# Kernel optimization log

Hardware: AMD Instinct MI355X
Metric: run time of the kernel (lower is better)

The kernel has to match this reference:

```python
import jax, jax.numpy as jnp
import numpy as np

N = 100000   # num nodes
E = 1600000  # num edges (before self loops)
D = 128      # feature / hidden dim
H = 256      # mlp hidden
L = 40       # num labels


def setup_inputs() -> dict:
    key = jax.random.key(0)
    ks = jax.random.split(key, 12)
    x = jax.random.normal(ks[0], (N, D), dtype=jnp.float32)
    edge_index = jax.random.randint(ks[1], (2, E), 0, N, dtype=jnp.int32)
    def glorot(k, shape):
        lim = float(np.sqrt(6.0 / (shape[0] + shape[1])))
        return jax.random.uniform(k, shape, jnp.float32, -lim, lim)
    params = {
        "W0": glorot(ks[2], (D, D)), "b0": jnp.zeros((D,), jnp.float32),
        "W1": glorot(ks[3], (D, D)), "b1": jnp.zeros((D,), jnp.float32),
        "W2": glorot(ks[4], (D, D)), "b2": jnp.zeros((D,), jnp.float32),
        "Wm1": glorot(ks[5], (D, H)), "bm1": jnp.zeros((H,), jnp.float32),
        "Wm2": glorot(ks[6], (H, L)), "bm2": jnp.zeros((L,), jnp.float32),
    }
    return {"x": x, "edge_index": edge_index, **params}


def _gcn_norm(edge_index):
    # add self loops (renorm trick), symmetric normalization D^-1/2 A D^-1/2
    self_loops = jnp.arange(N, dtype=edge_index.dtype)
    row = jnp.concatenate([edge_index[0], self_loops])
    col = jnp.concatenate([edge_index[1], self_loops])
    ones = jnp.ones(row.shape[0], jnp.float32)
    deg = jax.ops.segment_sum(ones, row, num_segments=N)
    dinv = jnp.where(deg > 0, jax.lax.rsqrt(deg), 0.0)
    norm_w = dinv[row] * dinv[col]  # [E+N]
    return row, col, norm_w


def _sage_layer(x, row, col, norm_w, W, b):
    msg = x[col] * norm_w[:, None]                      # [E+N, D] gather
    agg = jax.ops.segment_sum(msg, row, num_segments=N)  # [N, D] scatter-add
    return jax.nn.relu(agg @ W + b)


def reference(x, edge_index, W0, b0, W1, b1, W2, b2, Wm1, bm1, Wm2, bm2):
    row, col, norm_w = _gcn_norm(edge_index)
    h = _sage_layer(x, row, col, norm_w, W0, b0)
    h = _sage_layer(h, row, col, norm_w, W1, b1)
    h = _sage_layer(h, row, col, norm_w, W2, b2)
    h = jax.nn.relu(h @ Wm1 + bm1)  # Flatten is identity on [N, D]
    return h @ Wm2 + bm2            # [N, L] logits
```

## Files before the change

kernel.cpp:

```cpp
#include <hip/hip_runtime.h>
#include <hip/hip_bf16.h>
#include <stdint.h>

#define NN 100000
#define NE 1600000
#define DD 128
#define HH 256
#define LL 40

typedef __attribute__((ext_vector_type(8))) short short8;
typedef __attribute__((ext_vector_type(4))) float float4v;

__device__ __forceinline__ float bfu_lo(uint32_t u){ union{uint32_t i;float f;}v; v.i=u<<16; return v.f; }
__device__ __forceinline__ float bfu_hi(uint32_t u){ union{uint32_t i;float f;}v; v.i=u&0xFFFF0000u; return v.f; }
__device__ __forceinline__ float bf2f(uint16_t u){ union{uint32_t i;float f;}v; v.i=((uint32_t)u)<<16; return v.f; }
__device__ __forceinline__ uint16_t f2bf(float f){
  union{float f;uint32_t i;}v; v.f=f; uint32_t u=v.i;
  u += 0x7FFFu + ((u>>16)&1u); return (uint16_t)(u>>16);
}
__device__ __forceinline__ void split2(float f, short &hi, short &lo){
  uint16_t h = f2bf(f);
  hi = (short)h;
  lo = (short)f2bf(f - bf2f(h));
}
__device__ __forceinline__ float u2f(uint32_t u){ union{uint32_t i;float f;}v; v.i=u; return v.f; }


__global__ __launch_bounds__(256) void count_edges(const int* __restrict__ row,
                                                   int* __restrict__ counts, uint16_t* __restrict__ rank){
  int e = blockIdx.x*256 + threadIdx.x;
  if (e < NE) rank[e] = (uint16_t)atomicAdd(&counts[row[e]], 1);
}

__global__ __launch_bounds__(256) void scan_partial(const int* __restrict__ counts,
                                                    int* __restrict__ offs, int* __restrict__ bsums,
                                                    float* __restrict__ dinv){
  __shared__ int sh[256];
  int t = threadIdx.x, i = blockIdx.x*256 + t;
  int v = (i < NN) ? counts[i] : 0;
  if (i < NN) dinv[i] = rsqrtf((float)(v + 1));
  sh[t] = v; __syncthreads();
  for (int d = 1; d < 256; d <<= 1){
    int x = (t >= d) ? sh[t-d] : 0;
    __syncthreads();
    sh[t] += x;
    __syncthreads();
  }
  if (i < NN) offs[i] = sh[t] - v;
  if (t == 255) bsums[blockIdx.x] = sh[255];
}

__global__ __launch_bounds__(512) void scan_block(int* __restrict__ bsums, int nb){
  __shared__ int sh[512];
  int t = threadIdx.x;
  int v = (t < nb) ? bsums[t] : 0;
  sh[t] = v; __syncthreads();
  for (int d = 1; d < 512; d <<= 1){
    int x = (t >= d) ? sh[t-d] : 0;
    __syncthreads();
    sh[t] += x;
    __syncthreads();
  }
  if (t < nb) bsums[t] = sh[t] - v;
}

__global__ __launch_bounds__(256) void scan_add(int* __restrict__ offs, const int* __restrict__ bsums){
  int i = blockIdx.x*256 + threadIdx.x;
  if (i < NN) offs[i] += bsums[blockIdx.x];
  if (i == 0) offs[NN] = NE;
}

__global__ __launch_bounds__(256) void fill_csr(const int* __restrict__ row, const int* __restrict__ col,
                                                const uint16_t* __restrict__ rank,
                                                const int* __restrict__ offs,
                                                const float* __restrict__ dinv,
                                                uint2* __restrict__ csr_cw){
  int e = blockIdx.x*256 + threadIdx.x;
  if (e < NE){
    int r = row[e];
    int c = col[e];
    int p = offs[r] + (int)rank[e];
    uint2 v;
    v.x = (uint32_t)c;
    union{float f;uint32_t i;}w; w.f = dinv[c];
    v.y = w.i;
    csr_cw[p] = v;
  }
}

__global__ __launch_bounds__(256) void cvt_bf16(const float2* __restrict__ x, uint32_t* __restrict__ hb){
  int i = blockIdx.x*256 + threadIdx.x;
  if (i < NN*64){
    float2 v = x[i];
    hb[i] = (uint32_t)f2bf(v.x) | ((uint32_t)f2bf(v.y) << 16);
  }
}


template<int KDIM, int NCOL, int NTBP>
__global__ __launch_bounds__(256) void swz(const float* __restrict__ W, uint16_t* __restrict__ Wf){
  constexpr int KB = KDIM / 32;
  constexpr int TOT = KB * NTBP * 512;
  int idx = blockIdx.x*256 + threadIdx.x;
  if (idx >= TOT) return;
  int frag = idx >> 9, r = idx & 511, ln = r >> 3, j = r & 7;
  int kb = frag / NTBP, nt = frag - kb*NTBP;
  int k = kb*32 + ((ln >> 4) << 3) + j;
  int n = nt*16 + (ln & 15);
  float w = (n < NCOL) ? W[k*NCOL + n] : 0.f;
  Wf[idx] = f2bf(w);
}


__global__ __launch_bounds__(256) void agg_gemm(const uint32_t* __restrict__ hb,
                                                const int* __restrict__ offs,
                                                const uint2* __restrict__ csr_cw,
                                                const float* __restrict__ dinv,
                                                const uint16_t* __restrict__ Wf,
                                                const float* __restrict__ bias,
                                                uint16_t* __restrict__ Hout){
  __shared__ float lds[16*129];
  const int lane = threadIdx.x & 63;
  const int wid = threadIdx.x >> 6;
  const int rbase = blockIdx.x*16;

  for (int rl = wid*4; rl < wid*4 + 4; ++rl){
    const int w = rbase + rl;
    const int s = offs[w], e = offs[w+1];
    const float dr = dinv[w];
    const uint32_t us = hb[(size_t)w*64 + lane];

    float a0=0.f,a1=0.f,b0=0.f,b1=0.f,c0=0.f,c1=0.f,d0=0.f,d1=0.f;
    float e0=0.f,e1=0.f,f0=0.f,f1=0.f,g0=0.f,g1=0.f,h0=0.f,h1=0.f;
    int i = s;
    for (; i + 8 <= e; i += 8){
      uint2 p0=csr_cw[i],  p1=csr_cw[i+1], p2=csr_cw[i+2], p3=csr_cw[i+3];
      uint2 p4=csr_cw[i+4],p5=csr_cw[i+5], p6=csr_cw[i+6], p7=csr_cw[i+7];
      uint32_t u0=hb[(size_t)p0.x*64+lane], u1=hb[(size_t)p1.x*64+lane];
      uint32_t u2=hb[(size_t)p2.x*64+lane], u3=hb[(size_t)p3.x*64+lane];
      uint32_t u4=hb[(size_t)p4.x*64+lane], u5=hb[(size_t)p5.x*64+lane];
      uint32_t u6=hb[(size_t)p6.x*64+lane], u7=hb[(size_t)p7.x*64+lane];
      a0 += u2f(p0.y)*bfu_lo(u0); a1 += u2f(p0.y)*bfu_hi(u0);
      b0 += u2f(p1.y)*bfu_lo(u1); b1 += u2f(p1.y)*bfu_hi(u1);
      c0 += u2f(p2.y)*bfu_lo(u2); c1 += u2f(p2.y)*bfu_hi(u2);
      d0 += u2f(p3.y)*bfu_lo(u3); d1 += u2f(p3.y)*bfu_hi(u3);
      e0 += u2f(p4.y)*bfu_lo(u4); e1 += u2f(p4.y)*bfu_hi(u4);
      f0 += u2f(p5.y)*bfu_lo(u5); f1 += u2f(p5.y)*bfu_hi(u5);
      g0 += u2f(p6.y)*bfu_lo(u6); g1 += u2f(p6.y)*bfu_hi(u6);
      h0 += u2f(p7.y)*bfu_lo(u7); h1 += u2f(p7.y)*bfu_hi(u7);
    }
    if (i + 4 <= e){
      uint2 p0=csr_cw[i], p1=csr_cw[i+1], p2=csr_cw[i+2], p3=csr_cw[i+3];
      uint32_t u0=hb[(size_t)p0.x*64+lane], u1=hb[(size_t)p1.x*64+lane];
      uint32_t u2=hb[(size_t)p2.x*64+lane], u3=hb[(size_t)p3.x*64+lane];
      a0 += u2f(p0.y)*bfu_lo(u0); a1 += u2f(p0.y)*bfu_hi(u0);
      b0 += u2f(p1.y)*bfu_lo(u1); b1 += u2f(p1.y)*bfu_hi(u1);
      c0 += u2f(p2.y)*bfu_lo(u2); c1 += u2f(p2.y)*bfu_hi(u2);
      d0 += u2f(p3.y)*bfu_lo(u3); d1 += u2f(p3.y)*bfu_hi(u3);
      i += 4;
    }
    for (; i < e; ++i){
      uint2 p = csr_cw[i];
      uint32_t u = hb[(size_t)p.x*64 + lane];
      a0 += u2f(p.y)*bfu_lo(u); a1 += u2f(p.y)*bfu_hi(u);
    }
    float r0 = (((a0+b0)+(c0+d0)) + ((e0+f0)+(g0+h0))) + dr*bfu_lo(us);
    float r1 = (((a1+b1)+(c1+d1)) + ((e1+f1)+(g1+h1))) + dr*bfu_hi(us);
    lds[rl*129 + 2*lane]     = r0*dr;
    lds[rl*129 + 2*lane + 1] = r1*dr;
  }
  __syncthreads();

  const int mr = lane & 15;
  const int ko = (lane >> 4) << 3;
  float4v acc[2];
  { float4v z = {0.f,0.f,0.f,0.f}; acc[0] = z; acc[1] = z; }
#pragma unroll
  for (int kb = 0; kb < 4; ++kb){
    short8 ah, al;
#pragma unroll
    for (int j = 0; j < 8; ++j){
      float f = lds[mr*129 + kb*32 + ko + j];
      short h, l; split2(f, h, l); ah[j] = h; al[j] = l;
    }
#pragma unroll
    for (int t = 0; t < 2; ++t){
      int nt = wid*2 + t;
      short8 bf = *(const short8*)&Wf[(kb*8 + nt)*512 + lane*8];
      acc[t] = __builtin_amdgcn_mfma_f32_16x16x32_bf16(ah, bf, acc[t], 0, 0, 0);
      acc[t] = __builtin_amdgcn_mfma_f32_16x16x32_bf16(al, bf, acc[t], 0, 0, 0);
    }
  }
  const int col = lane & 15;
  const int rb  = (lane >> 4) * 4;
#pragma unroll
  for (int t = 0; t < 2; ++t){
    int n = (wid*2 + t)*16 + col;
    float bv = bias[n];
#pragma unroll
    for (int r = 0; r < 4; ++r){
      int m = rbase + rb + r;
      float v = acc[t][r] + bv;
      Hout[(size_t)m*128 + n] = f2bf(v > 0.f ? v : 0.f);
    }
  }
}


#define HS 260

__global__ __launch_bounds__(256) void mlp_fused(const uint16_t* __restrict__ Hb,
                                                 const uint16_t* __restrict__ W1f,
                                                 const float* __restrict__ b1,
                                                 const uint16_t* __restrict__ W2f,
                                                 const float* __restrict__ b2,
                                                 float* __restrict__ out, int M){
  __shared__ uint16_t hid[128*HS];
  const int lane = threadIdx.x & 63;
  const int wid = threadIdx.x >> 6;
  const int mbase = blockIdx.x*128 + wid*32;
  const int mr = lane & 15;
  const int a0r = (mbase + mr < M) ? (mbase + mr) : (M-1);
  const int a1r = (mbase + 16 + mr < M) ? (mbase + 16 + mr) : (M-1);
  const int ko = (lane >> 4) << 3;
  const int col = lane & 15;
  const int rb  = (lane >> 4) * 4;

  float4v acc1[16][2];
#pragma unroll
  for (int nt = 0; nt < 16; ++nt){ float4v z = {0.f,0.f,0.f,0.f}; acc1[nt][0] = z; acc1[nt][1] = z; }
#pragma unroll
  for (int kb = 0; kb < 4; ++kb){
    short8 af0 = *(const short8*)&Hb[(size_t)a0r*128 + kb*32 + ko];
    short8 af1 = *(const short8*)&Hb[(size_t)a1r*128 + kb*32 + ko];
#pragma unroll
    for (int nt = 0; nt < 16; ++nt){
      short8 bf = *(const short8*)&W1f[(kb*16 + nt)*512 + lane*8];
      acc1[nt][0] = __builtin_amdgcn_mfma_f32_16x16x32_bf16(af0, bf, acc1[nt][0], 0, 0, 0);
      acc1[nt][1] = __builtin_amdgcn_mfma_f32_16x16x32_bf16(af1, bf, acc1[nt][1], 0, 0, 0);
    }
  }
#pragma unroll
  for (int nt = 0; nt < 16; ++nt){
    float bv = b1[nt*16 + col];
#pragma unroll
    for (int mt = 0; mt < 2; ++mt){
#pragma unroll
      for (int r = 0; r < 4; ++r){
        float v = acc1[nt][mt][r] + bv;
        v = v > 0.f ? v : 0.f;
        hid[(wid*32 + mt*16 + rb + r)*HS + nt*16 + col] = f2bf(v);
      }
    }
  }
  __syncthreads();

  float4v acc2[3][2];
#pragma unroll
  for (int nt = 0; nt < 3; ++nt){ float4v z = {0.f,0.f,0.f,0.f}; acc2[nt][0] = z; acc2[nt][1] = z; }
#pragma unroll
  for (int kb = 0; kb < 8; ++kb){
    short8 a0 = *(const short8*)&hid[(wid*32 + mr)*HS + kb*32 + ko];
    short8 a1 = *(const short8*)&hid[(wid*32 + 16 + mr)*HS + kb*32 + ko];
#pragma unroll
    for (int nt = 0; nt < 3; ++nt){
      short8 bf = *(const short8*)&W2f[(kb*3 + nt)*512 + lane*8];
      acc2[nt][0] = __builtin_amdgcn_mfma_f32_16x16x32_bf16(a0, bf, acc2[nt][0], 0, 0, 0);
      acc2[nt][1] = __builtin_amdgcn_mfma_f32_16x16x32_bf16(a1, bf, acc2[nt][1], 0, 0, 0);
    }
  }
#pragma unroll
  for (int nt = 0; nt < 3; ++nt){
    int n = nt*16 + col;
    if (n < LL){
      float bv = b2[n];
#pragma unroll
      for (int mt = 0; mt < 2; ++mt){
#pragma unroll
        for (int r = 0; r < 4; ++r){
          int m = mbase + mt*16 + rb + r;
          if (m < M) out[(size_t)m*LL + n] = acc2[nt][mt][r] + bv;
        }
      }
    }
  }
}


extern "C" void kernel_launch(void* const* d_in, const int* in_sizes, int n_in,
                              void* d_out, int out_size, void* d_ws, size_t ws_size,
                              hipStream_t stream){
  const float* x   = (const float*)d_in[0];
  const int*   ei  = (const int*)d_in[1];
  const float* W0  = (const float*)d_in[2];
  const float* b0  = (const float*)d_in[3];
  const float* W1  = (const float*)d_in[4];
  const float* b1  = (const float*)d_in[5];
  const float* W2  = (const float*)d_in[6];
  const float* b2  = (const float*)d_in[7];
  const float* Wm1 = (const float*)d_in[8];
  const float* bm1 = (const float*)d_in[9];
  const float* Wm2 = (const float*)d_in[10];
  const float* bm2 = (const float*)d_in[11];
  const int* row = ei;
  const int* col = ei + NE;

  char* ws = (char*)d_ws;
  size_t off = 0;
  auto alloc = [&](size_t bytes)->void*{
    void* p = ws + off;
    off += (bytes + 255) & ~(size_t)255;
    return p;
  };
  int*      counts  = (int*)alloc((size_t)NN*4);
  int*      offs    = (int*)alloc(((size_t)NN+1)*4);
  int*      bsums   = (int*)alloc(1024*4);
  float*    dinv    = (float*)alloc((size_t)NN*4);
  uint16_t* rank    = (uint16_t*)alloc((size_t)NE*2);
  uint2*    csr_cw  = (uint2*)alloc((size_t)NE*8);
  uint16_t* W0f     = (uint16_t*)alloc(4*8*512*2);
  uint16_t* W1f     = (uint16_t*)alloc(4*8*512*2);
  uint16_t* W2f     = (uint16_t*)alloc(4*8*512*2);
  uint16_t* Wm1f    = (uint16_t*)alloc(4*16*512*2);
  uint16_t* Wm2f    = (uint16_t*)alloc(8*3*512*2);
  uint16_t* hb      = (uint16_t*)alloc((size_t)NN*DD*2);
  uint16_t* hb2     = (uint16_t*)alloc((size_t)NN*DD*2);

  hipMemsetAsync(counts, 0, (size_t)NN*4, stream);
  count_edges<<<(NE+255)/256, 256, 0, stream>>>(row, counts, rank);
  const int NB = (NN+255)/256;
  scan_partial<<<NB, 256, 0, stream>>>(counts, offs, bsums, dinv);
  scan_block<<<1, 512, 0, stream>>>(bsums, NB);
  scan_add<<<NB, 256, 0, stream>>>(offs, bsums);
  fill_csr<<<(NE+255)/256, 256, 0, stream>>>(row, col, rank, offs, dinv, csr_cw);

  swz<128,128,8><<<(4*8*512+255)/256, 256, 0, stream>>>(W0, W0f);
  swz<128,128,8><<<(4*8*512+255)/256, 256, 0, stream>>>(W1, W1f);
  swz<128,128,8><<<(4*8*512+255)/256, 256, 0, stream>>>(W2, W2f);
  swz<128,256,16><<<(4*16*512+255)/256, 256, 0, stream>>>(Wm1, Wm1f);
  swz<256,40,3><<<(8*3*512+255)/256, 256, 0, stream>>>(Wm2, Wm2f);

  cvt_bf16<<<(NN*64+255)/256, 256, 0, stream>>>((const float2*)x, (uint32_t*)hb);

  const int LB = NN/16;

  agg_gemm<<<LB, 256, 0, stream>>>((const uint32_t*)hb,  offs, csr_cw, dinv, W0f, b0, hb2);
  agg_gemm<<<LB, 256, 0, stream>>>((const uint32_t*)hb2, offs, csr_cw, dinv, W1f, b1, hb);
  agg_gemm<<<LB, 256, 0, stream>>>((const uint32_t*)hb,  offs, csr_cw, dinv, W2f, b2, hb2);

  const int GB128 = (NN + 127)/128;
  mlp_fused<<<GB128, 256, 0, stream>>>(hb2, Wm1f, bm1, Wm2f, bm2, (float*)d_out, NN);
}
```

Measured before the change: 507.5 us.

## Fuse prep kernels, pair edges per thread, and dynamically assign rows in aggregation

Merges the counts memset, the bf16 conversion of x and the five weight swizzle kernels into one prep launch to cut launch overhead. count_edges and fill_csr now handle two edges per thread with vectorized int2/ushort2 loads. agg_gemm replaces the fixed four-rows-per-wave split with an LDS atomic ticket, so waves pull rows dynamically and degree imbalance between rows is spread more evenly. The ticket adds one atomic and one shuffle per row.

```diff
diff --git a/kernel.cpp b/kernel.cpp
--- a/kernel.cpp
+++ b/kernel.cpp
@@ -26,10 +26,61 @@
 __device__ __forceinline__ float u2f(uint32_t u){ union{uint32_t i;float f;}v; v.i=u; return v.f; }
 
 
+__device__ __forceinline__ void swz_one(const float* __restrict__ W, uint16_t* __restrict__ Wf,
+                                        int idx, int NCOL, int NTBP){
+  int frag = idx >> 9, r = idx & 511, ln = r >> 3, j = r & 7;
+  int kb = frag / NTBP, nt = frag - kb*NTBP;
+  int k = kb*32 + ((ln >> 4) << 3) + j;
+  int n = nt*16 + (ln & 15);
+  float w = (n < NCOL) ? W[k*NCOL + n] : 0.f;
+  Wf[idx] = f2bf(w);
+}
+
+#define PREP_CVT   (NN)
+#define PREP_W0    (PREP_CVT + NN*64)
+#define PREP_W1    (PREP_W0 + 16384)
+#define PREP_W2    (PREP_W1 + 16384)
+#define PREP_WM1   (PREP_W2 + 16384)
+#define PREP_WM2   (PREP_WM1 + 32768)
+#define PREP_TOT   (PREP_WM2 + 12288)
+
+__global__ __launch_bounds__(256) void prep(const float2* __restrict__ x,
+                                            int* __restrict__ counts, uint32_t* __restrict__ hb,
+                                            const float* __restrict__ W0, uint16_t* __restrict__ W0f,
+                                            const float* __restrict__ W1, uint16_t* __restrict__ W1f,
+                                            const float* __restrict__ W2, uint16_t* __restrict__ W2f,
+                                            const float* __restrict__ Wm1, uint16_t* __restrict__ Wm1f,
+                                            const float* __restrict__ Wm2, uint16_t* __restrict__ Wm2f){
+  int idx = blockIdx.x*256 + threadIdx.x;
+  if (idx < PREP_CVT){
+    counts[idx] = 0;
+  } else if (idx < PREP_W0){
+    int i = idx - PREP_CVT;
+    float2 v = x[i];
+    hb[i] = (uint32_t)f2bf(v.x) | ((uint32_t)f2bf(v.y) << 16);
+  } else if (idx < PREP_W1){
+    swz_one(W0, W0f, idx - PREP_W0, 128, 8);
+  } else if (idx < PREP_W2){
+    swz_one(W1, W1f, idx - PREP_W1, 128, 8);
+  } else if (idx < PREP_WM1){
+    swz_one(W2, W2f, idx - PREP_W2, 128, 8);
+  } else if (idx < PREP_WM2){
+    swz_one(Wm1, Wm1f, idx - PREP_WM1, 256, 16);
+  } else if (idx < PREP_TOT){
+    swz_one(Wm2, Wm2f, idx - PREP_WM2, 40, 3);
+  }
+}
+
+
 __global__ __launch_bounds__(256) void count_edges(const int* __restrict__ row,
                                                    int* __restrict__ counts, uint16_t* __restrict__ rank){
-  int e = blockIdx.x*256 + threadIdx.x;
-  if (e < NE) rank[e] = (uint16_t)atomicAdd(&counts[row[e]], 1);
+  int e2 = blockIdx.x*256 + threadIdx.x;
+  if (e2 < NE/2){
+    int2 r2 = ((const int2*)row)[e2];
+    uint16_t a = (uint16_t)atomicAdd(&counts[r2.x], 1);
+    uint16_t b = (uint16_t)atomicAdd(&counts[r2.y], 1);
+    ((ushort2*)rank)[e2] = make_ushort2(a, b);
+  }
 }
 
 __global__ __launch_bounds__(256) void scan_partial(const int* __restrict__ counts,
@@ -75,40 +126,21 @@
                                                 const int* __restrict__ offs,
                                                 const float* __restrict__ dinv,
                                                 uint2* __restrict__ csr_cw){
-  int e = blockIdx.x*256 + threadIdx.x;
-  if (e < NE){
-    int r = row[e];
-    int c = col[e];
-    int p = offs[r] + (int)rank[e];
-    uint2 v;
-    v.x = (uint32_t)c;
-    union{float f;uint32_t i;}w; w.f = dinv[c];
-    v.y = w.i;
-    csr_cw[p] = v;
-  }
-}
-
-__global__ __launch_bounds__(256) void cvt_bf16(const float2* __restrict__ x, uint32_t* __restrict__ hb){
-  int i = blockIdx.x*256 + threadIdx.x;
-  if (i < NN*64){
-    float2 v = x[i];
-    hb[i] = (uint32_t)f2bf(v.x) | ((uint32_t)f2bf(v.y) << 16);
-  }
-}
-
-
-template<int KDIM, int NCOL, int NTBP>
-__global__ __launch_bounds__(256) void swz(const float* __restrict__ W, uint16_t* __restrict__ Wf){
-  constexpr int KB = KDIM / 32;
-  constexpr int TOT = KB * NTBP * 512;
-  int idx = blockIdx.x*256 + threadIdx.x;
-  if (idx >= TOT) return;
-  int frag = idx >> 9, r = idx & 511, ln = r >> 3, j = r & 7;
-  int kb = frag / NTBP, nt = frag - kb*NTBP;
-  int k = kb*32 + ((ln >> 4) << 3) + j;
-  int n = nt*16 + (ln & 15);
-  float w = (n < NCOL) ? W[k*NCOL + n] : 0.f;
-  Wf[idx] = f2bf(w);
+  int e2 = blockIdx.x*256 + threadIdx.x;
+  if (e2 < NE/2){
+    int2 r2 = ((const int2*)row)[e2];
+    int2 c2 = ((const int2*)col)[e2];
+    ushort2 k2 = ((const ushort2*)rank)[e2];
+    int p0 = offs[r2.x] + (int)k2.x;
+    int p1 = offs[r2.y] + (int)k2.y;
+    uint2 v0, v1;
+    v0.x = (uint32_t)c2.x;
+    v1.x = (uint32_t)c2.y;
+    union{float f;uint32_t i;}w0; w0.f = dinv[c2.x]; v0.y = w0.i;
+    union{float f;uint32_t i;}w1; w1.f = dinv[c2.y]; v1.y = w1.i;
+    csr_cw[p0] = v0;
+    csr_cw[p1] = v1;
+  }
 }
 
 
@@ -120,11 +152,18 @@
                                                 const float* __restrict__ bias,
                                                 uint16_t* __restrict__ Hout){
   __shared__ float lds[16*129];
+  __shared__ int ticket;
   const int lane = threadIdx.x & 63;
-  const int wid = threadIdx.x >> 6;
   const int rbase = blockIdx.x*16;
-
-  for (int rl = wid*4; rl < wid*4 + 4; ++rl){
+  if (threadIdx.x == 0) ticket = 0;
+  __syncthreads();
+
+  for (;;){
+    int rl;
+    if (lane == 0) rl = atomicAdd(&ticket, 1);
+    rl = __shfl(rl, 0);
+    if (rl >= 16) break;
+
     const int w = rbase + rl;
     const int s = offs[w], e = offs[w+1];
     const float dr = dinv[w];
@@ -171,6 +210,7 @@
   }
   __syncthreads();
 
+  const int wid = threadIdx.x >> 6;
   const int mr = lane & 15;
   const int ko = (lane >> 4) << 3;
   float4v acc[2];
@@ -326,21 +366,14 @@
   uint16_t* hb      = (uint16_t*)alloc((size_t)NN*DD*2);
   uint16_t* hb2     = (uint16_t*)alloc((size_t)NN*DD*2);
 
-  hipMemsetAsync(counts, 0, (size_t)NN*4, stream);
-  count_edges<<<(NE+255)/256, 256, 0, stream>>>(row, counts, rank);
+  prep<<<(PREP_TOT+255)/256, 256, 0, stream>>>((const float2*)x, counts, (uint32_t*)hb,
+                                               W0, W0f, W1, W1f, W2, W2f, Wm1, Wm1f, Wm2, Wm2f);
+  count_edges<<<(NE/2+255)/256, 256, 0, stream>>>(row, counts, rank);
   const int NB = (NN+255)/256;
   scan_partial<<<NB, 256, 0, stream>>>(counts, offs, bsums, dinv);
   scan_block<<<1, 512, 0, stream>>>(bsums, NB);
   scan_add<<<NB, 256, 0, stream>>>(offs, bsums);
-  fill_csr<<<(NE+255)/256, 256, 0, stream>>>(row, col, rank, offs, dinv, csr_cw);
-
-  swz<128,128,8><<<(4*8*512+255)/256, 256, 0, stream>>>(W0, W0f);
-  swz<128,128,8><<<(4*8*512+255)/256, 256, 0, stream>>>(W1, W1f);
-  swz<128,128,8><<<(4*8*512+255)/256, 256, 0, stream>>>(W2, W2f);
-  swz<128,256,16><<<(4*16*512+255)/256, 256, 0, stream>>>(Wm1, Wm1f);
-  swz<256,40,3><<<(8*3*512+255)/256, 256, 0, stream>>>(Wm2, Wm2f);
-
-  cvt_bf16<<<(NN*64+255)/256, 256, 0, stream>>>((const float2*)x, (uint32_t*)hb);
+  fill_csr<<<(NE/2+255)/256, 256, 0, stream>>>(row, col, rank, offs, dinv, csr_cw);
 
   const int LB = NN/16;
 
```

Measured after the change: 505.5 us. About the same (-0.4%).
